# Kernel optimization log

Hardware: AMD Instinct MI355X
Metric: run time of the kernel (lower is better)

The kernel has to match this reference:

```python
import jax, jax.numpy as jnp
import numpy as np


def conv2d(x, w, b, pad):
    out = jax.lax.conv_general_dilated(x, w, (1, 1), ((pad, pad), (pad, pad)),
                                       dimension_numbers=('NCHW', 'OIHW', 'NCHW'))
    return out + b[None, :, None, None]


def silu(x):
    return x * jax.nn.sigmoid(x)


def group_norm(x, g, b, groups, eps=1e-5):
    B, C, H, W = x.shape
    xg = x.reshape(B, groups, C // groups, H, W)
    m = xg.mean(axis=(2, 3, 4), keepdims=True)
    v = xg.var(axis=(2, 3, 4), keepdims=True)
    xg = (xg - m) * jax.lax.rsqrt(v + eps)
    return xg.reshape(B, C, H, W) * g[None, :, None, None] + b[None, :, None, None]


def snake_cumsum(off):
    # off: [B,K,H,W]. Center kernel point has zero offset; points accumulate
    # outward from center (the 'snake' bend), as in DSCNet.
    K = off.shape[1]
    c = K // 2
    upper = jnp.cumsum(off[:, c + 1:], axis=1)
    lower = jnp.flip(jnp.cumsum(jnp.flip(off[:, :c], axis=1), axis=1), axis=1)
    return jnp.concatenate([lower, jnp.zeros_like(off[:, :1]), upper], axis=1)


def bilinear_gather(img, ys, xs):
    # img [B,C,H,W]; ys,xs [B,K,H,W] float coords -> sampled [B,C,K,H,W]
    B, C, H, W = img.shape
    K = ys.shape[1]
    ys = jnp.clip(ys, 0.0, H - 1.0)
    xs = jnp.clip(xs, 0.0, W - 1.0)
    y0f = jnp.floor(ys)
    x0f = jnp.floor(xs)
    wy = (ys - y0f)[:, None]  # [B,1,K,H,W]
    wx = (xs - x0f)[:, None]
    y0 = y0f.astype(jnp.int32)
    x0 = x0f.astype(jnp.int32)
    y1 = jnp.minimum(y0 + 1, H - 1)
    x1 = jnp.minimum(x0 + 1, W - 1)
    flat = img.reshape(B, C, H * W)

    def gat(yi, xi):
        idx = (yi * W + xi).reshape(B, -1)  # [B, K*H*W]
        g = jnp.take_along_axis(flat, idx[:, None, :], axis=2)
        return g.reshape(B, C, K, H, W)

    return (gat(y0, x0) * (1 - wy) * (1 - wx) + gat(y0, x1) * (1 - wy) * wx
            + gat(y1, x0) * wy * (1 - wx) + gat(y1, x1) * wy * wx)


def dsconv(x, off_w, off_b, dsc_w, dsc_b, gn_g, gn_b, morph, extend_scope=1.0):
    # Dynamic snake conv for one morphology.
    # morph 0: kernel spreads along x, bends in y; morph 1: opposite.
    B, C, H, W = x.shape
    K = dsc_w.shape[-1]
    c = K // 2
    off = jnp.tanh(conv2d(x, off_w, off_b, pad=1))  # [B,2K,H,W]; BN folded into conv bias
    bend = snake_cumsum(off[:, :K] if morph == 0 else off[:, K:])  # [B,K,H,W]
    spread = (jnp.arange(K) - c).astype(x.dtype)[None, :, None, None]
    hh = jnp.arange(H, dtype=x.dtype)[None, None, :, None]
    ww = jnp.arange(W, dtype=x.dtype)[None, None, None, :]
    if morph == 0:
        ys = hh + extend_scope * bend
        xs = jnp.broadcast_to(ww + spread, ys.shape)
    else:
        xs = ww + extend_scope * bend
        ys = jnp.broadcast_to(hh + spread, xs.shape)
    sampled = bilinear_gather(x, ys, xs)  # [B,C,K,H,W]
    # k-point conv over the stacked snake axis == (K,1)/(1,K) conv with stride K
    out = jnp.einsum('bckhw,ock->bohw', sampled, dsc_w) + dsc_b[None, :, None, None]
    O = dsc_w.shape[0]
    return jax.nn.relu(group_norm(out, gn_g, gn_b, groups=O // 4))


def dysnake_conv(x, p):
    # DySnakeConv: standard conv + snake-x + snake-y, concat, 1x1 fuse
    kpad = p['conv0_w'].shape[-1] // 2
    a = silu(conv2d(x, p['conv0_w'], p['conv0_b'], pad=kpad))
    bx = dsconv(x, p['offx_w'], p['offx_b'], p['dscx_w'], p['dscx_b'], p['gnx_g'], p['gnx_b'], morph=0)
    by = dsconv(x, p['offy_w'], p['offy_b'], p['dscy_w'], p['dscy_b'], p['gny_g'], p['gny_b'], morph=1)
    cat = jnp.concatenate([a, bx, by], axis=1)  # [B,3*ouc,H,W]
    return silu(jnp.einsum('bchw,oc->bohw', cat, p['fuse_w']) + p['fuse_b'][None, :, None, None])


_PNAMES = ['conv0_w', 'conv0_b', 'offx_w', 'offx_b', 'dscx_w', 'dscx_b', 'gnx_g', 'gnx_b',
           'offy_w', 'offy_b', 'dscy_w', 'dscy_b', 'gny_g', 'gny_b', 'fuse_w', 'fuse_b']


def setup_inputs() -> dict:
    key = jax.random.key(0)
    ks = iter(jax.random.split(key, 64))

    def rn(shape, s=0.05):
        return jax.random.normal(next(ks), shape, dtype=jnp.float32) * s

    B, H, W = 8, 80, 80
    c1, c2, c_ = 256, 256, 128
    kk = 3

    def block(inc, ouc, pre):
        return {
            pre + 'conv0_w': rn((ouc, inc, kk, kk)), pre + 'conv0_b': rn((ouc,)),
            pre + 'offx_w': rn((2 * kk, inc, 3, 3)), pre + 'offx_b': rn((2 * kk,)),
            pre + 'dscx_w': rn((ouc, inc, kk)), pre + 'dscx_b': rn((ouc,)),
            pre + 'gnx_g': jnp.ones((ouc,), jnp.float32), pre + 'gnx_b': jnp.zeros((ouc,), jnp.float32),
            pre + 'offy_w': rn((2 * kk, inc, 3, 3)), pre + 'offy_b': rn((2 * kk,)),
            pre + 'dscy_w': rn((ouc, inc, kk)), pre + 'dscy_b': rn((ouc,)),
            pre + 'gny_g': jnp.ones((ouc,), jnp.float32), pre + 'gny_b': jnp.zeros((ouc,), jnp.float32),
            pre + 'fuse_w': rn((ouc, 3 * ouc)), pre + 'fuse_b': rn((ouc,)),
        }

    inp = {'x': jax.random.normal(next(ks), (B, c1, H, W), dtype=jnp.float32)}
    inp.update(block(c1, c_, 'cv1_'))
    inp.update(block(c_, c2, 'cv2_'))
    return inp


def reference(x, cv1_conv0_w, cv1_conv0_b, cv1_offx_w, cv1_offx_b, cv1_dscx_w, cv1_dscx_b,
              cv1_gnx_g, cv1_gnx_b, cv1_offy_w, cv1_offy_b, cv1_dscy_w, cv1_dscy_b,
              cv1_gny_g, cv1_gny_b, cv1_fuse_w, cv1_fuse_b,
              cv2_conv0_w, cv2_conv0_b, cv2_offx_w, cv2_offx_b, cv2_dscx_w, cv2_dscx_b,
              cv2_gnx_g, cv2_gnx_b, cv2_offy_w, cv2_offy_b, cv2_dscy_w, cv2_dscy_b,
              cv2_gny_g, cv2_gny_b, cv2_fuse_w, cv2_fuse_b):
    p1 = dict(zip(_PNAMES, (cv1_conv0_w, cv1_conv0_b, cv1_offx_w, cv1_offx_b, cv1_dscx_w, cv1_dscx_b,
                            cv1_gnx_g, cv1_gnx_b, cv1_offy_w, cv1_offy_b, cv1_dscy_w, cv1_dscy_b,
                            cv1_gny_g, cv1_gny_b, cv1_fuse_w, cv1_fuse_b)))
    p2 = dict(zip(_PNAMES, (cv2_conv0_w, cv2_conv0_b, cv2_offx_w, cv2_offx_b, cv2_dscx_w, cv2_dscx_b,
                            cv2_gnx_g, cv2_gnx_b, cv2_offy_w, cv2_offy_b, cv2_dscy_w, cv2_dscy_b,
                            cv2_gny_g, cv2_gny_b, cv2_fuse_w, cv2_fuse_b)))
    h = dysnake_conv(x, p1)
    h = dysnake_conv(h, p2)
    return x + h  # shortcut and c1 == c2
```

## Files before the change

kernel.cpp:

```cpp
#include <hip/hip_runtime.h>
#include <cstddef>

#define B_   8
#define H_   80
#define W_   80
#define HW   6400

typedef __attribute__((ext_vector_type(8)))  short short8;
typedef __attribute__((ext_vector_type(16))) float f32x16;

__device__ __forceinline__ float bf2f(ushort u) {
    return __uint_as_float(((unsigned)u) << 16);
}
__device__ __forceinline__ ushort f2bf(float f) {
    unsigned u = __float_as_uint(f);
    u += 0x7FFF + ((u >> 16) & 1);
    return (ushort)(u >> 16);
}
__device__ __forceinline__ f32x16 mfma16(short8 a, short8 b, f32x16 c) {
    return __builtin_amdgcn_mfma_f32_32x32x16_bf16(a, b, c, 0, 0, 0);
}
__device__ __forceinline__ void async16(const void* g, void* l) {
    __builtin_amdgcn_global_load_lds(
        (const __attribute__((address_space(1))) unsigned int*)g,
        (__attribute__((address_space(3))) unsigned int*)l, 16, 0, 0);
}
__device__ __forceinline__ const ushort* frag_ptr(const ushort* sbuf, int row, int c8l) {
    return sbuf + row * 64 + ((c8l ^ (row & 7)) << 3);
}

__global__ __launch_bounds__(256) void transpose_x_kernel(
    const float* __restrict__ x, ushort* __restrict__ xh, int C) {
    __shared__ float s[64][65];
    int hw0 = blockIdx.x * 64, c0 = blockIdx.y * 64, b = blockIdx.z;
    int t = threadIdx.x;
    int hl = t & 63, cq = t >> 6;
    #pragma unroll
    for (int i = 0; i < 16; i++) {
        int cl = cq * 16 + i;
        s[cl][hl] = x[((size_t)(b * C + c0 + cl)) * HW + hw0 + hl];
    }
    __syncthreads();
    int cl = t & 63, hq = t >> 6;
    #pragma unroll
    for (int i = 0; i < 16; i++) {
        int hl2 = hq * 16 + i;
        xh[((size_t)(b * HW + hw0 + hl2)) * C + c0 + cl] = f2bf(s[cl][hl2]);
    }
}

__global__ __launch_bounds__(256) void final_add_kernel(
    const float* __restrict__ x, const ushort* __restrict__ h2,
    float* __restrict__ out, int C) {
    __shared__ float s[64][65];
    int hw0 = blockIdx.x * 64, c0 = blockIdx.y * 64, b = blockIdx.z;
    int t = threadIdx.x;
    int cl = t & 63, hq = t >> 6;
    #pragma unroll
    for (int i = 0; i < 16; i++) {
        int hl = hq * 16 + i;
        s[cl][hl] = bf2f(h2[((size_t)(b * HW + hw0 + hl)) * C + c0 + cl]);
    }
    __syncthreads();
    int hl = t & 63, cq = t >> 6;
    #pragma unroll
    for (int i = 0; i < 16; i++) {
        int cl2 = cq * 16 + i;
        size_t o = ((size_t)(b * C + c0 + cl2)) * HW + hw0 + hl;
        out[o] = x[o] + s[cl2][hl];
    }
}

__global__ void wprep_kernel(const float* __restrict__ src,
                             ushort* __restrict__ dst, int OC, int CIN, int T) {
    int idx = blockIdx.x * 256 + threadIdx.x;
    if (idx >= OC * CIN * T) return;
    int oc = idx / (CIN * T);
    int r = idx - oc * CIN * T;
    int ci = r / T, t_ = r - ci * T;
    dst[((size_t)oc * T + t_) * CIN + ci] = f2bf(src[idx]);
}

__global__ void wprep_off_kernel(const float* __restrict__ wx_,
                                 const float* __restrict__ bx_,
                                 const float* __restrict__ wy_,
                                 const float* __restrict__ by_,
                                 ushort* __restrict__ dst,
                                 float* __restrict__ bdst, int CIN) {
    int idx = blockIdx.x * 256 + threadIdx.x;
    if (idx < 4) {
        const int chs[4] = {0, 2, 3, 5};
        bdst[idx] = (idx < 2) ? bx_[chs[idx]] : by_[chs[idx]];
    }
    if (idx >= 32 * 9 * CIN) return;
    int oc = idx / (9 * CIN);
    int r = idx - oc * 9 * CIN;
    int tap = r / CIN, ci = r - tap * CIN;
    float v = 0.f;
    if (oc < 4) {
        const int chs[4] = {0, 2, 3, 5};
        const float* src = (oc < 2) ? wx_ : wy_;
        v = src[((size_t)chs[oc] * CIN + ci) * 9 + tap];
    }
    dst[idx] = f2bf(v);
}

__global__ __launch_bounds__(256, 2) void off_conv_mfma_kernel(
    const ushort* __restrict__ xh, const ushort* __restrict__ wB,
    const float* __restrict__ bias, float* __restrict__ off4, int CIN) {
    __shared__ ushort s_x[162 * 64];
    __shared__ ushort s_w[144 * 64];
    int tid = threadIdx.x;
    int ty0 = (blockIdx.x / 5) * 16, tx0 = (blockIdx.x % 5) * 16;
    int b = blockIdx.y;
    int lane = tid & 63, wid = tid >> 6;
    int l31 = lane & 31, kg = lane >> 5;
    int pym[2], pxm[2];
    #pragma unroll
    for (int mf = 0; mf < 2; mf++) {
        int p = wid * 64 + mf * 32 + l31;
        pym[mf] = p >> 4; pxm[mf] = p & 15;
    }
    f32x16 acc[2] = {};
    for (int c0 = 0; c0 < CIN; c0 += 32) {
        __syncthreads();
        for (int u = tid; u < 1296; u += 256) {
            int pid = u >> 2, ci8 = u & 3;
            int r = pid / 18, c = pid - r * 18;
            int gy = ty0 + r - 1, gx = tx0 + c - 1;
            uint4 v = make_uint4(0, 0, 0, 0);
            if ((unsigned)gy < H_ && (unsigned)gx < W_)
                v = *(const uint4*)(xh + ((size_t)(b * HW + gy * W_ + gx)) * CIN + c0 + ci8 * 8);
            int row = pid >> 1;
            int phys = (((pid & 1) << 2) + ci8) ^ (row & 7);
            *(uint4*)(s_x + row * 64 + phys * 8) = v;
        }
        for (int cc = wid; cc < 18; cc += 4) {
            int L = cc * 64 + lane;
            int row = L >> 3, phys = L & 7;
            int logical = phys ^ (row & 7);
            int tap = row >> 4, ocp = row & 15;
            int oc = ocp * 2 + (logical >> 2), ci8 = logical & 3;
            async16(wB + ((size_t)oc * 9 + tap) * CIN + c0 + ci8 * 8,
                    s_w + (size_t)L * 8);
        }
        __syncthreads();
        #pragma unroll
        for (int tap = 0; tap < 9; tap++) {
            int dy = tap / 3, dx = tap - dy * 3;
            int wrow = tap * 16 + (l31 >> 1);
            #pragma unroll
            for (int ks = 0; ks < 2; ks++) {
                int blk = ks * 2 + kg;
                int wphys = (((l31 & 1) << 2) + blk) ^ (wrow & 7);
                short8 bfr = *(const short8*)(s_w + wrow * 64 + wphys * 8);
                #pragma unroll
                for (int mf = 0; mf < 2; mf++) {
                    int pix = (pym[mf] + dy) * 18 + (pxm[mf] + dx);
                    int xrow = pix >> 1;
                    int xphys = (((pix & 1) << 2) + blk) ^ (xrow & 7);
                    short8 afr = *(const short8*)(s_x + xrow * 64 + xphys * 8);
                    acc[mf] = mfma16(afr, bfr, acc[mf]);
                }
            }
        }
    }
    int oc = l31;
    if (oc < 4) {
        float bb = bias[oc];
        #pragma unroll
        for (int mf = 0; mf < 2; mf++) {
            #pragma unroll
            for (int reg = 0; reg < 16; reg++) {
                int row = (reg & 3) + 8 * (reg >> 2) + 4 * kg;
                int p = wid * 64 + mf * 32 + row;
                int y = ty0 + (p >> 4), x = tx0 + (p & 15);
                off4[((size_t)b * 4 + oc) * HW + y * W_ + x] = tanhf(acc[mf][reg] + bb);
            }
        }
    }
}

__global__ __launch_bounds__(256, 2) void conv3x3_mfma_kernel(
    const ushort* __restrict__ xh, const ushort* __restrict__ wB,
    const float* __restrict__ bias, ushort* __restrict__ out,
    int CIN, int OC) {
    __shared__ ushort s_x[162 * 64];
    __shared__ ushort s_w[288 * 64];
    int tid = threadIdx.x;
    int ty0 = (blockIdx.x / 5) * 16, tx0 = (blockIdx.x % 5) * 16;
    int n0 = blockIdx.y * 64, b = blockIdx.z;
    int lane = tid & 63, wid = tid >> 6;
    int l31 = lane & 31, kg = lane >> 5;
    int wm = wid >> 1, wn = wid & 1;
    int pym[4], pxm[4];
    #pragma unroll
    for (int mf = 0; mf < 4; mf++) {
        int p = wm * 128 + mf * 32 + l31;
        pym[mf] = p >> 4; pxm[mf] = p & 15;
    }
    f32x16 acc[4] = {};
    for (int c0 = 0; c0 < CIN; c0 += 32) {
        __syncthreads();
        for (int u = tid; u < 1296; u += 256) {
            int pid = u >> 2, ci8 = u & 3;
            int r = pid / 18, c = pid - r * 18;
            int gy = ty0 + r - 1, gx = tx0 + c - 1;
            uint4 v = make_uint4(0, 0, 0, 0);
            if ((unsigned)gy < H_ && (unsigned)gx < W_)
                v = *(const uint4*)(xh + ((size_t)(b * HW + gy * W_ + gx)) * CIN + c0 + ci8 * 8);
            int row = pid >> 1;
            int phys = (((pid & 1) << 2) + ci8) ^ (row & 7);
            *(uint4*)(s_x + row * 64 + phys * 8) = v;
        }
        #pragma unroll
        for (int j = 0; j < 9; j++) {
            int L = (wid * 9 + j) * 64 + lane;
            int row = L >> 3, phys = L & 7;
            int logical = phys ^ (row & 7);
            int tap = row >> 5, ocp = row & 31;
            int oc = ocp * 2 + (logical >> 2), ci8 = logical & 3;
            async16(wB + ((size_t)(n0 + oc) * 9 + tap) * CIN + c0 + ci8 * 8,
                    s_w + (size_t)L * 8);
        }
        __syncthreads();
        #pragma unroll
        for (int tap = 0; tap < 9; tap++) {
            int dy = tap / 3, dx = tap - dy * 3;
            int ocl = wn * 32 + l31;
            int wrow = tap * 32 + (ocl >> 1);
            #pragma unroll
            for (int ks = 0; ks < 2; ks++) {
                int blk = ks * 2 + kg;
                int wphys = (((ocl & 1) << 2) + blk) ^ (wrow & 7);
                short8 bfr = *(const short8*)(s_w + wrow * 64 + wphys * 8);
                #pragma unroll
                for (int mf = 0; mf < 4; mf++) {
                    int pix = (pym[mf] + dy) * 18 + (pxm[mf] + dx);
                    int xrow = pix >> 1;
                    int xphys = (((pix & 1) << 2) + blk) ^ (xrow & 7);
                    short8 afr = *(const short8*)(s_x + xrow * 64 + xphys * 8);
                    acc[mf] = mfma16(afr, bfr, acc[mf]);
                }
            }
        }
    }
    int oc = n0 + wn * 32 + l31;
    float bb = bias[oc];
    #pragma unroll
    for (int mf = 0; mf < 4; mf++) {
        #pragma unroll
        for (int reg = 0; reg < 16; reg++) {
            int row = (reg & 3) + 8 * (reg >> 2) + 4 * kg;
            int p = wm * 128 + mf * 32 + row;
            int y = ty0 + (p >> 4), x = tx0 + (p & 15);
            float v = acc[mf][reg] + bb;
            v = v / (1.f + expf(-v));
            out[((size_t)(b * HW + y * W_ + x)) * OC + oc] = f2bf(v);
        }
    }
}

__global__ __launch_bounds__(256, 4) void dsc_gemm_kernel(
    const ushort* __restrict__ xh, const float* __restrict__ off4,
    const ushort* __restrict__ Bwx, const float* __restrict__ biasx,
    ushort* __restrict__ outx,
    const ushort* __restrict__ Bwy, const float* __restrict__ biasy,
    ushort* __restrict__ outy, float* __restrict__ stat, int CIN, int OC) {
    __shared__ ushort s_a[128 * 64];
    __shared__ ushort s_b[128 * 64];
    __shared__ int   s_i0[3][128];
    __shared__ int   s_i1[3][128];
    __shared__ float s_wl[3][128];
    int tid = threadIdx.x;
    int morph = blockIdx.z;
    const ushort* Bw = morph ? Bwy : Bwx;
    const float* bias = morph ? biasy : biasx;
    ushort* out = morph ? outy : outx;
    float* statm = stat + (size_t)morph * B_ * 256 * 2;
    int m0 = blockIdx.x * 128, n0 = blockIdx.y * 128;
    int b = m0 / HW, hw0 = m0 - b * HW;
    for (int u = tid; u < 384; u += 256) {
        int k3 = u >> 7, r = u & 127;
        int hw = hw0 + r;
        int h = hw / W_, w = hw - h * W_;
        float bend = 0.f;
        if (k3 != 1) {
            int mp = (morph ? 2 : 0) + (k3 >> 1);
            bend = off4[((size_t)b * 4 + mp) * HW + hw];
        }
        int i0, i1; float wl;
        if (morph == 0) {
            float ys = fminf(fmaxf((float)h + bend, 0.f), 79.f);
            float y0f = floorf(ys); wl = ys - y0f;
            int y0 = (int)y0f, y1 = min(y0 + 1, 79);
            int xk = min(max(w + k3 - 1, 0), 79);
            i0 = y0 * W_ + xk; i1 = y1 * W_ + xk;
        } else {
            float xs = fminf(fmaxf((float)w + bend, 0.f), 79.f);
            float x0f = floorf(xs); wl = xs - x0f;
            int x0 = (int)x0f, x1 = min(x0 + 1, 79);
            int yk = min(max(h + k3 - 1, 0), 79);
            i0 = yk * W_ + x0; i1 = yk * W_ + x1;
        }
        s_i0[k3][r] = i0; s_i1[k3][r] = i1; s_wl[k3][r] = wl;
    }
    int lane = tid & 63, wid = tid >> 6;
    int l31 = lane & 31, kg = lane >> 5;
    int wm = wid >> 1, wn = wid & 1;
    f32x16 acc[2][2] = {};
    int K = 3 * CIN, nk = K >> 6;
    const ushort* xb = xh + (size_t)b * HW * CIN;
    for (int kc = 0; kc < nk; kc++) {
        int kg64 = kc << 6;
        int k3 = kg64 / CIN;
        int cioff = kg64 - k3 * CIN;
        __syncthreads();
        #pragma unroll
        for (int j = 0; j < 4; j++) {
            int s = (wid * 4 + j) * 64 + lane;
            int r = s >> 3, c8p = s & 7;
            int c8l = c8p ^ (r & 7);
            async16(Bw + (size_t)(n0 + r) * K + kg64 + c8l * 8, s_b + s * 8);
        }
        #pragma unroll
        for (int i = 0; i < 4; i++) {
            int s = i * 256 + tid;
            int r = s >> 3, c8p = s & 7;
            int c8l = c8p ^ (r & 7);
            int ci = cioff + c8l * 8;
            float wl = s_wl[k3][r];
            uint4 u0 = *(const uint4*)(xb + (size_t)s_i0[k3][r] * CIN + ci);
            uint4 u1 = *(const uint4*)(xb + (size_t)s_i1[k3][r] * CIN + ci);
            const ushort* p0 = (const ushort*)&u0;
            const ushort* p1 = (const ushort*)&u1;
            ushort tv[8];
            #pragma unroll
            for (int j = 0; j < 8; j++) {
                float f0 = bf2f(p0[j]);
                tv[j] = f2bf(f0 + (bf2f(p1[j]) - f0) * wl);
            }
            *(uint4*)(s_a + s * 8) = *(uint4*)tv;
        }
        __syncthreads();
        #pragma unroll
        for (int ks = 0; ks < 4; ks++) {
            int c8l = ks * 2 + kg;
            short8 af0 = *(const short8*)frag_ptr(s_a, wm * 64 + l31, c8l);
            short8 af1 = *(const short8*)frag_ptr(s_a, wm * 64 + 32 + l31, c8l);
            short8 bf0 = *(const short8*)frag_ptr(s_b, wn * 64 + l31, c8l);
            short8 bf1 = *(const short8*)frag_ptr(s_b, wn * 64 + 32 + l31, c8l);
            acc[0][0] = mfma16(af0, bf0, acc[0][0]);
            acc[0][1] = mfma16(af0, bf1, acc[0][1]);
            acc[1][0] = mfma16(af1, bf0, acc[1][0]);
            acc[1][1] = mfma16(af1, bf1, acc[1][1]);
        }
    }
    #pragma unroll
    for (int nf = 0; nf < 2; nf++) {
        int n = n0 + wn * 64 + nf * 32 + l31;
        float bb = bias[n];
        float ssum = 0.f, ssq = 0.f;
        #pragma unroll
        for (int mf = 0; mf < 2; mf++) {
            #pragma unroll
            for (int reg = 0; reg < 16; reg++) {
                int row = (reg & 3) + 8 * (reg >> 2) + 4 * kg;
                int m = m0 + wm * 64 + mf * 32 + row;
                float v = acc[mf][nf][reg] + bb;
                ssum += v; ssq += v * v;
                out[(size_t)m * OC + n] = f2bf(v);
            }
        }
        ssum += __shfl_xor(ssum, 32);
        ssq  += __shfl_xor(ssq, 32);
        if (kg == 0) {
            float* st = statm + ((size_t)b * OC + n) * 2;
            atomicAdd(st, ssum);
            atomicAdd(st + 1, ssq);
        }
    }
}

__global__ __launch_bounds__(256, 4) void gemm128_kernel(
    const ushort* __restrict__ a0, const ushort* __restrict__ a1,
    const ushort* __restrict__ a2, int part_k,
    const ushort* __restrict__ Bw, int K, int N,
    const float* __restrict__ bias, ushort* __restrict__ out, int epi_silu) {
    __shared__ ushort s_a[128 * 64];
    __shared__ ushort s_b[128 * 64];
    int tid = threadIdx.x;
    int m0 = blockIdx.x * 128, n0 = blockIdx.y * 128;
    int lane = tid & 63, wid = tid >> 6;
    int l31 = lane & 31, kg = lane >> 5;
    int wm = wid >> 1, wn = wid & 1;
    f32x16 acc[2][2] = {};
    int nk = K >> 6;
    for (int kc = 0; kc < nk; kc++) {
        int kg64 = kc << 6;
        int part = kg64 / part_k;
        int koff = kg64 - part * part_k;
        const ushort* ap = (part == 0) ? a0 : (part == 1 ? a1 : a2);
        __syncthreads();
        #pragma unroll
        for (int j = 0; j < 4; j++) {
            int s = (wid * 4 + j) * 64 + lane;
            int r = s >> 3, c8p = s & 7;
            int c8l = c8p ^ (r & 7);
            async16(ap + (size_t)(m0 + r) * part_k + koff + c8l * 8, s_a + s * 8);
            async16(Bw + (size_t)(n0 + r) * K + kg64 + c8l * 8, s_b + s * 8);
        }
        __syncthreads();
        #pragma unroll
        for (int ks = 0; ks < 4; ks++) {
            int c8l = ks * 2 + kg;
            short8 af0 = *(const short8*)frag_ptr(s_a, wm * 64 + l31, c8l);
            short8 af1 = *(const short8*)frag_ptr(s_a, wm * 64 + 32 + l31, c8l);
            short8 bf0 = *(const short8*)frag_ptr(s_b, wn * 64 + l31, c8l);
            short8 bf1 = *(const short8*)frag_ptr(s_b, wn * 64 + 32 + l31, c8l);
            acc[0][0] = mfma16(af0, bf0, acc[0][0]);
            acc[0][1] = mfma16(af0, bf1, acc[0][1]);
            acc[1][0] = mfma16(af1, bf0, acc[1][0]);
            acc[1][1] = mfma16(af1, bf1, acc[1][1]);
        }
    }
    #pragma unroll
    for (int nf = 0; nf < 2; nf++) {
        int n = n0 + wn * 64 + nf * 32 + l31;
        float bb = bias[n];
        #pragma unroll
        for (int mf = 0; mf < 2; mf++) {
            #pragma unroll
            for (int reg = 0; reg < 16; reg++) {
                int row = (reg & 3) + 8 * (reg >> 2) + 4 * kg;
                int m = m0 + wm * 64 + mf * 32 + row;
                float v = acc[mf][nf][reg] + bb;
                if (epi_silu) v = v / (1.f + expf(-v));
                out[(size_t)m * N + n] = f2bf(v);
            }
        }
    }
}

__global__ void gn_finalize_kernel(const float* __restrict__ stat,
                                   const float* __restrict__ gx,
                                   const float* __restrict__ bx,
                                   const float* __restrict__ gy,
                                   const float* __restrict__ by,
                                   float* __restrict__ scx, float* __restrict__ shx,
                                   float* __restrict__ scy, float* __restrict__ shy,
                                   int C) {
    int idx = blockIdx.x * 256 + threadIdx.x;
    if (idx >= B_ * C) return;
    int which = blockIdx.y;
    const float* gamma = which ? gy : gx;
    const float* beta  = which ? by : bx;
    float* sc = which ? scy : scx;
    float* sh = which ? shy : shx;
    int b = idx / C, c = idx - b * C;
    const float* st = stat + (size_t)which * B_ * 256 * 2
                    + ((size_t)b * C + (c & ~3)) * 2;
    float s  = st[0] + st[2] + st[4] + st[6];
    float sq = st[1] + st[3] + st[5] + st[7];
    float mean = s / (4.f * HW);
    float var = sq / (4.f * HW) - mean * mean;
    float rs = rsqrtf(var + 1e-5f);
    float scale = rs * gamma[c];
    sc[idx] = scale;
    sh[idx] = beta[c] - mean * scale;
}

__global__ __launch_bounds__(256) void gn_apply_kernel(
    ushort* __restrict__ bqx, ushort* __restrict__ bqy,
    const float* __restrict__ scx, const float* __restrict__ shx,
    const float* __restrict__ scy, const float* __restrict__ shy, int C) {
    ushort* bq = blockIdx.y ? bqy : bqx;
    const float* sc = blockIdx.y ? scy : scx;
    const float* sh = blockIdx.y ? shy : shx;
    size_t e = ((size_t)blockIdx.x * 256 + threadIdx.x) * 8;
    int c = (int)(e % C);
    int b = (int)(e / ((size_t)HW * C));
    const float* scb = sc + (size_t)b * C + c;
    const float* shb = sh + (size_t)b * C + c;
    uint4 v = *(const uint4*)(bq + e);
    const ushort* sv = (const ushort*)&v;
    ushort tv[8];
    #pragma unroll
    for (int j = 0; j < 8; j++)
        tv[j] = f2bf(fmaxf(bf2f(sv[j]) * scb[j] + shb[j], 0.f));
    *(uint4*)(bq + e) = *(uint4*)tv;
}

struct BlkBuf {
    ushort *xh, *abuf, *bqx, *bqy, *hout;
    float *off4, *stat, *scx, *shx, *scy, *shy, *boff;
    ushort *wc, *wdx, *wdy, *wf, *woff;
};

static void run_block(const BlkBuf& B, int CIN, int OC,
                      const float* const* P, hipStream_t stream) {
    dim3 blk(256);
    hipMemsetAsync(B.stat, 0, (size_t)2 * B_ * 256 * 2 * 4, stream);
    off_conv_mfma_kernel<<<dim3(25, B_), blk, 0, stream>>>(
        B.xh, B.woff, B.boff, B.off4, CIN);
    conv3x3_mfma_kernel<<<dim3(25, OC / 64, B_), blk, 0, stream>>>(
        B.xh, B.wc, P[1], B.abuf, CIN, OC);
    dsc_gemm_kernel<<<dim3(400, OC / 128, 2), blk, 0, stream>>>(
        B.xh, B.off4, B.wdx, P[5], B.bqx, B.wdy, P[11], B.bqy, B.stat, CIN, OC);
    int fgrid = (B_ * OC + 255) / 256;
    gn_finalize_kernel<<<dim3(fgrid, 2), blk, 0, stream>>>(
        B.stat, P[6], P[7], P[12], P[13], B.scx, B.shx, B.scy, B.shy, OC);
    gn_apply_kernel<<<dim3((B_ * HW * OC) / 2048, 2), blk, 0, stream>>>(
        B.bqx, B.bqy, B.scx, B.shx, B.scy, B.shy, OC);
    gemm128_kernel<<<dim3(400, OC / 128), blk, 0, stream>>>(
        B.abuf, B.bqx, B.bqy, OC, B.wf, 3 * OC, OC, P[15], B.hout, 1);
}

extern "C" void kernel_launch(void* const* d_in, const int* in_sizes, int n_in,
                              void* d_out, int out_size, void* d_ws, size_t ws_size,
                              hipStream_t stream) {
    const float* x = (const float*)d_in[0];
    const float* P1[16];
    const float* P2[16];
    for (int i = 0; i < 16; i++) {
        P1[i] = (const float*)d_in[1 + i];
        P2[i] = (const float*)d_in[17 + i];
    }
    char* base = (char*)d_ws;
    size_t off = 0;
    auto alloc = [&](size_t bytes) -> char* {
        off = (off + 255) & ~(size_t)255;
        char* p = base + off;
        off += bytes;
        return p;
    };
    ushort* xh   = (ushort*)alloc((size_t)B_ * HW * 256 * 2);
    ushort* abuf = (ushort*)alloc((size_t)B_ * HW * 256 * 2);
    ushort* bqx  = (ushort*)alloc((size_t)B_ * HW * 256 * 2);
    ushort* bqy  = (ushort*)alloc((size_t)B_ * HW * 256 * 2);
    ushort* h1   = (ushort*)alloc((size_t)B_ * HW * 128 * 2);
    float*  off4 = (float*)alloc((size_t)B_ * 4 * HW * 4);
    float*  stat = (float*)alloc((size_t)2 * B_ * 256 * 2 * 4);
    float*  scx  = (float*)alloc(B_ * 256 * 4);
    float*  shx  = (float*)alloc(B_ * 256 * 4);
    float*  scy  = (float*)alloc(B_ * 256 * 4);
    float*  shy  = (float*)alloc(B_ * 256 * 4);
    ushort* wc1  = (ushort*)alloc((size_t)128 * 9 * 256 * 2);
    ushort* wc2  = (ushort*)alloc((size_t)256 * 9 * 128 * 2);
    ushort* wdx1 = (ushort*)alloc((size_t)128 * 3 * 256 * 2);
    ushort* wdy1 = (ushort*)alloc((size_t)128 * 3 * 256 * 2);
    ushort* wdx2 = (ushort*)alloc((size_t)256 * 3 * 128 * 2);
    ushort* wdy2 = (ushort*)alloc((size_t)256 * 3 * 128 * 2);
    ushort* wf1  = (ushort*)alloc((size_t)128 * 384 * 2);
    ushort* wf2  = (ushort*)alloc((size_t)256 * 768 * 2);
    ushort* wo1  = (ushort*)alloc((size_t)32 * 9 * 256 * 2);
    ushort* wo2  = (ushort*)alloc((size_t)32 * 9 * 128 * 2);
    float*  bo1  = (float*)alloc(32 * 4);
    float*  bo2  = (float*)alloc(32 * 4);

    dim3 blk(256);
    auto wp = [&](const float* s, ushort* d, int OC, int CIN, int T) {
        int n = OC * CIN * T;
        wprep_kernel<<<(n + 255) / 256, blk, 0, stream>>>(s, d, OC, CIN, T);
    };
    wp(P1[0], wc1, 128, 256, 9);
    wp(P1[4], wdx1, 128, 256, 3);
    wp(P1[10], wdy1, 128, 256, 3);
    wp(P1[14], wf1, 128, 384, 1);
    wp(P2[0], wc2, 256, 128, 9);
    wp(P2[4], wdx2, 256, 128, 3);
    wp(P2[10], wdy2, 256, 128, 3);
    wp(P2[14], wf2, 256, 768, 1);
    wprep_off_kernel<<<(32 * 9 * 256 + 255) / 256, blk, 0, stream>>>(
        P1[2], P1[3], P1[8], P1[9], wo1, bo1, 256);
    wprep_off_kernel<<<(32 * 9 * 128 + 255) / 256, blk, 0, stream>>>(
        P2[2], P2[3], P2[8], P2[9], wo2, bo2, 128);

    transpose_x_kernel<<<dim3(100, 4, B_), blk, 0, stream>>>(x, xh, 256);

    BlkBuf B1 = {xh, abuf, bqx, bqy, h1, off4, stat, scx, shx, scy, shy,
                 bo1, wc1, wdx1, wdy1, wf1, wo1};
    run_block(B1, 256, 128, P1, stream);

    ushort* h2 = xh;
    BlkBuf B2 = {h1, abuf, bqx, bqy, h2, off4, stat, scx, shx, scy, shy,
                 bo2, wc2, wdx2, wdy2, wf2, wo2};
    run_block(B2, 128, 256, P2, stream);

    final_add_kernel<<<dim3(100, 4, B_), blk, 0, stream>>>(x, h2, (float*)d_out, 256);
}
```

Before: 572.2 us.

## Zero-pad NHWC activations and run conv3x3 as implicit GEMM with async loads

Activations are stored in a zero-padded 82x82 NHWC buffer so convolution halo loads need no bounds checks. The 3x3 conv is rewritten as a 128x128 implicit GEMM that streams both operands straight into LDS with global_load_lds over a 9*CIN reduction, replacing the spatial-tile kernel that reused one input halo across all taps. Producer kernels write into the padded interior, and two memsets clear the borders. The trade-off is that input tiles are reloaded once per tap instead of being reused from shared memory, and the buffers grow slightly.

```diff
diff --git a/kernel.cpp b/kernel.cpp
--- a/kernel.cpp
+++ b/kernel.cpp
@@ -5,6 +5,8 @@
 #define H_   80
 #define W_   80
 #define HW   6400
+#define W2   82
+#define HW2  6724
 
 typedef __attribute__((ext_vector_type(8)))  short short8;
 typedef __attribute__((ext_vector_type(16))) float f32x16;
@@ -30,7 +32,7 @@
 }
 
 __global__ __launch_bounds__(256) void transpose_x_kernel(
-    const float* __restrict__ x, ushort* __restrict__ xh, int C) {
+    const float* __restrict__ x, ushort* __restrict__ xp, int C) {
     __shared__ float s[64][65];
     int hw0 = blockIdx.x * 64, c0 = blockIdx.y * 64, b = blockIdx.z;
     int t = threadIdx.x;
@@ -45,7 +47,9 @@
     #pragma unroll
     for (int i = 0; i < 16; i++) {
         int hl2 = hq * 16 + i;
-        xh[((size_t)(b * HW + hw0 + hl2)) * C + c0 + cl] = f2bf(s[cl][hl2]);
+        int hw = hw0 + hl2;
+        int h = hw / W_, w = hw - h * W_;
+        xp[((size_t)(b * HW2 + (h + 1) * W2 + w + 1)) * C + c0 + cl] = f2bf(s[cl][hl2]);
     }
 }
 
@@ -106,7 +110,7 @@
 }
 
 __global__ __launch_bounds__(256, 2) void off_conv_mfma_kernel(
-    const ushort* __restrict__ xh, const ushort* __restrict__ wB,
+    const ushort* __restrict__ xp, const ushort* __restrict__ wB,
     const float* __restrict__ bias, float* __restrict__ off4, int CIN) {
     __shared__ ushort s_x[162 * 64];
     __shared__ ushort s_w[144 * 64];
@@ -127,10 +131,9 @@
         for (int u = tid; u < 1296; u += 256) {
             int pid = u >> 2, ci8 = u & 3;
             int r = pid / 18, c = pid - r * 18;
-            int gy = ty0 + r - 1, gx = tx0 + c - 1;
-            uint4 v = make_uint4(0, 0, 0, 0);
-            if ((unsigned)gy < H_ && (unsigned)gx < W_)
-                v = *(const uint4*)(xh + ((size_t)(b * HW + gy * W_ + gx)) * CIN + c0 + ci8 * 8);
+            int py = ty0 + r, px = tx0 + c;
+            uint4 v = *(const uint4*)(xp + ((size_t)(b * HW2 + py * W2 + px)) * CIN
+                                      + c0 + ci8 * 8);
             int row = pid >> 1;
             int phys = (((pid & 1) << 2) + ci8) ^ (row & 7);
             *(uint4*)(s_x + row * 64 + phys * 8) = v;
@@ -181,88 +184,81 @@
     }
 }
 
-__global__ __launch_bounds__(256, 2) void conv3x3_mfma_kernel(
-    const ushort* __restrict__ xh, const ushort* __restrict__ wB,
+__global__ __launch_bounds__(256, 4) void conv3x3_gemm_kernel(
+    const ushort* __restrict__ xp, const ushort* __restrict__ wB,
     const float* __restrict__ bias, ushort* __restrict__ out,
     int CIN, int OC) {
-    __shared__ ushort s_x[162 * 64];
-    __shared__ ushort s_w[288 * 64];
+    __shared__ ushort s_a[128 * 64];
+    __shared__ ushort s_b[128 * 64];
     int tid = threadIdx.x;
-    int ty0 = (blockIdx.x / 5) * 16, tx0 = (blockIdx.x % 5) * 16;
-    int n0 = blockIdx.y * 64, b = blockIdx.z;
+    int m0 = blockIdx.x * 128, n0 = blockIdx.y * 128;
+    int b = m0 / HW, hw0 = m0 - b * HW;
     int lane = tid & 63, wid = tid >> 6;
     int l31 = lane & 31, kg = lane >> 5;
     int wm = wid >> 1, wn = wid & 1;
-    int pym[4], pxm[4];
-    #pragma unroll
-    for (int mf = 0; mf < 4; mf++) {
-        int p = wm * 128 + mf * 32 + l31;
-        pym[mf] = p >> 4; pxm[mf] = p & 15;
-    }
-    f32x16 acc[4] = {};
-    for (int c0 = 0; c0 < CIN; c0 += 32) {
-        __syncthreads();
-        for (int u = tid; u < 1296; u += 256) {
-            int pid = u >> 2, ci8 = u & 3;
-            int r = pid / 18, c = pid - r * 18;
-            int gy = ty0 + r - 1, gx = tx0 + c - 1;
-            uint4 v = make_uint4(0, 0, 0, 0);
-            if ((unsigned)gy < H_ && (unsigned)gx < W_)
-                v = *(const uint4*)(xh + ((size_t)(b * HW + gy * W_ + gx)) * CIN + c0 + ci8 * 8);
-            int row = pid >> 1;
-            int phys = (((pid & 1) << 2) + ci8) ^ (row & 7);
-            *(uint4*)(s_x + row * 64 + phys * 8) = v;
-        }
-        #pragma unroll
-        for (int j = 0; j < 9; j++) {
-            int L = (wid * 9 + j) * 64 + lane;
-            int row = L >> 3, phys = L & 7;
-            int logical = phys ^ (row & 7);
-            int tap = row >> 5, ocp = row & 31;
-            int oc = ocp * 2 + (logical >> 2), ci8 = logical & 3;
-            async16(wB + ((size_t)(n0 + oc) * 9 + tap) * CIN + c0 + ci8 * 8,
-                    s_w + (size_t)L * 8);
-        }
-        __syncthreads();
-        #pragma unroll
-        for (int tap = 0; tap < 9; tap++) {
-            int dy = tap / 3, dx = tap - dy * 3;
-            int ocl = wn * 32 + l31;
-            int wrow = tap * 32 + (ocl >> 1);
+    const ushort* xpb = xp + (size_t)b * HW2 * CIN;
+    const ushort* asrc[4];
+    #pragma unroll
+    for (int j = 0; j < 4; j++) {
+        int s = (wid * 4 + j) * 64 + lane;
+        int r = s >> 3, c8p = s & 7;
+        int c8l = c8p ^ (r & 7);
+        int hw = hw0 + r;
+        int h = hw / W_, w = hw - h * W_;
+        asrc[j] = xpb + ((size_t)((h + 1) * W2 + (w + 1))) * CIN + c8l * 8;
+    }
+    f32x16 acc[2][2] = {};
+    int K = 9 * CIN, nk = K >> 6;
+    int tap = 0, cioff = 0;
+    for (int kc = 0; kc < nk; kc++) {
+        int kg64 = kc << 6;
+        int dy = tap / 3, dx = tap - dy * 3;
+        int soff = ((dy - 1) * W2 + (dx - 1)) * CIN + cioff;
+        __syncthreads();
+        #pragma unroll
+        for (int j = 0; j < 4; j++) {
+            int s = (wid * 4 + j) * 64 + lane;
+            int r = s >> 3, c8p = s & 7;
+            int c8l = c8p ^ (r & 7);
+            async16(wB + (size_t)(n0 + r) * K + kg64 + c8l * 8, s_b + s * 8);
+            async16(asrc[j] + soff, s_a + s * 8);
+        }
+        __syncthreads();
+        #pragma unroll
+        for (int ks = 0; ks < 4; ks++) {
+            int c8l = ks * 2 + kg;
+            short8 af0 = *(const short8*)frag_ptr(s_a, wm * 64 + l31, c8l);
+            short8 af1 = *(const short8*)frag_ptr(s_a, wm * 64 + 32 + l31, c8l);
+            short8 bf0 = *(const short8*)frag_ptr(s_b, wn * 64 + l31, c8l);
+            short8 bf1 = *(const short8*)frag_ptr(s_b, wn * 64 + 32 + l31, c8l);
+            acc[0][0] = mfma16(af0, bf0, acc[0][0]);
+            acc[0][1] = mfma16(af0, bf1, acc[0][1]);
+            acc[1][0] = mfma16(af1, bf0, acc[1][0]);
+            acc[1][1] = mfma16(af1, bf1, acc[1][1]);
+        }
+        cioff += 64;
+        if (cioff == CIN) { cioff = 0; tap++; }
+    }
+    #pragma unroll
+    for (int nf = 0; nf < 2; nf++) {
+        int n = n0 + wn * 64 + nf * 32 + l31;
+        float bb = bias[n];
+        #pragma unroll
+        for (int mf = 0; mf < 2; mf++) {
             #pragma unroll
-            for (int ks = 0; ks < 2; ks++) {
-                int blk = ks * 2 + kg;
-                int wphys = (((ocl & 1) << 2) + blk) ^ (wrow & 7);
-                short8 bfr = *(const short8*)(s_w + wrow * 64 + wphys * 8);
-                #pragma unroll
-                for (int mf = 0; mf < 4; mf++) {
-                    int pix = (pym[mf] + dy) * 18 + (pxm[mf] + dx);
-                    int xrow = pix >> 1;
-                    int xphys = (((pix & 1) << 2) + blk) ^ (xrow & 7);
-                    short8 afr = *(const short8*)(s_x + xrow * 64 + xphys * 8);
-                    acc[mf] = mfma16(afr, bfr, acc[mf]);
-                }
+            for (int reg = 0; reg < 16; reg++) {
+                int row = (reg & 3) + 8 * (reg >> 2) + 4 * kg;
+                int m = m0 + wm * 64 + mf * 32 + row;
+                float v = acc[mf][nf][reg] + bb;
+                v = v / (1.f + expf(-v));
+                out[(size_t)m * OC + n] = f2bf(v);
             }
         }
     }
-    int oc = n0 + wn * 32 + l31;
-    float bb = bias[oc];
-    #pragma unroll
-    for (int mf = 0; mf < 4; mf++) {
-        #pragma unroll
-        for (int reg = 0; reg < 16; reg++) {
-            int row = (reg & 3) + 8 * (reg >> 2) + 4 * kg;
-            int p = wm * 128 + mf * 32 + row;
-            int y = ty0 + (p >> 4), x = tx0 + (p & 15);
-            float v = acc[mf][reg] + bb;
-            v = v / (1.f + expf(-v));
-            out[((size_t)(b * HW + y * W_ + x)) * OC + oc] = f2bf(v);
-        }
-    }
 }
 
 __global__ __launch_bounds__(256, 4) void dsc_gemm_kernel(
-    const ushort* __restrict__ xh, const float* __restrict__ off4,
+    const ushort* __restrict__ xp, const float* __restrict__ off4,
     const ushort* __restrict__ Bwx, const float* __restrict__ biasx,
     ushort* __restrict__ outx,
     const ushort* __restrict__ Bwy, const float* __restrict__ biasy,
@@ -295,13 +291,13 @@
             float y0f = floorf(ys); wl = ys - y0f;
             int y0 = (int)y0f, y1 = min(y0 + 1, 79);
             int xk = min(max(w + k3 - 1, 0), 79);
-            i0 = y0 * W_ + xk; i1 = y1 * W_ + xk;
+            i0 = (y0 + 1) * W2 + xk + 1; i1 = (y1 + 1) * W2 + xk + 1;
         } else {
             float xs = fminf(fmaxf((float)w + bend, 0.f), 79.f);
             float x0f = floorf(xs); wl = xs - x0f;
             int x0 = (int)x0f, x1 = min(x0 + 1, 79);
             int yk = min(max(h + k3 - 1, 0), 79);
-            i0 = yk * W_ + x0; i1 = yk * W_ + x1;
+            i0 = (yk + 1) * W2 + x0 + 1; i1 = (yk + 1) * W2 + x1 + 1;
         }
         s_i0[k3][r] = i0; s_i1[k3][r] = i1; s_wl[k3][r] = wl;
     }
@@ -310,7 +306,7 @@
     int wm = wid >> 1, wn = wid & 1;
     f32x16 acc[2][2] = {};
     int K = 3 * CIN, nk = K >> 6;
-    const ushort* xb = xh + (size_t)b * HW * CIN;
+    const ushort* xb = xp + (size_t)b * HW2 * CIN;
     for (int kc = 0; kc < nk; kc++) {
         int kg64 = kc << 6;
         int k3 = kg64 / CIN;
@@ -386,7 +382,8 @@
     const ushort* __restrict__ a0, const ushort* __restrict__ a1,
     const ushort* __restrict__ a2, int part_k,
     const ushort* __restrict__ Bw, int K, int N,
-    const float* __restrict__ bias, ushort* __restrict__ out, int epi_silu) {
+    const float* __restrict__ bias, ushort* __restrict__ out, int epi_silu,
+    int out_pad) {
     __shared__ ushort s_a[128 * 64];
     __shared__ ushort s_b[128 * 64];
     int tid = threadIdx.x;
@@ -436,7 +433,13 @@
                 int m = m0 + wm * 64 + mf * 32 + row;
                 float v = acc[mf][nf][reg] + bb;
                 if (epi_silu) v = v / (1.f + expf(-v));
-                out[(size_t)m * N + n] = f2bf(v);
+                size_t mm = (size_t)m;
+                if (out_pad) {
+                    int bb_ = m / HW, hw = m - bb_ * HW;
+                    int h = hw / W_, w = hw - h * W_;
+                    mm = (size_t)bb_ * HW2 + (h + 1) * W2 + w + 1;
+                }
+                out[mm * N + n] = f2bf(v);
             }
         }
     }
@@ -492,28 +495,28 @@
 }
 
 struct BlkBuf {
-    ushort *xh, *abuf, *bqx, *bqy, *hout;
+    ushort *xp, *abuf, *bqx, *bqy, *hout;
     float *off4, *stat, *scx, *shx, *scy, *shy, *boff;
     ushort *wc, *wdx, *wdy, *wf, *woff;
 };
 
 static void run_block(const BlkBuf& B, int CIN, int OC,
-                      const float* const* P, hipStream_t stream) {
+                      const float* const* P, int out_pad, hipStream_t stream) {
     dim3 blk(256);
     hipMemsetAsync(B.stat, 0, (size_t)2 * B_ * 256 * 2 * 4, stream);
     off_conv_mfma_kernel<<<dim3(25, B_), blk, 0, stream>>>(
-        B.xh, B.woff, B.boff, B.off4, CIN);
-    conv3x3_mfma_kernel<<<dim3(25, OC / 64, B_), blk, 0, stream>>>(
-        B.xh, B.wc, P[1], B.abuf, CIN, OC);
+        B.xp, B.woff, B.boff, B.off4, CIN);
+    conv3x3_gemm_kernel<<<dim3(B_ * HW / 128, OC / 128), blk, 0, stream>>>(
+        B.xp, B.wc, P[1], B.abuf, CIN, OC);
     dsc_gemm_kernel<<<dim3(400, OC / 128, 2), blk, 0, stream>>>(
-        B.xh, B.off4, B.wdx, P[5], B.bqx, B.wdy, P[11], B.bqy, B.stat, CIN, OC);
+        B.xp, B.off4, B.wdx, P[5], B.bqx, B.wdy, P[11], B.bqy, B.stat, CIN, OC);
     int fgrid = (B_ * OC + 255) / 256;
     gn_finalize_kernel<<<dim3(fgrid, 2), blk, 0, stream>>>(
         B.stat, P[6], P[7], P[12], P[13], B.scx, B.shx, B.scy, B.shy, OC);
     gn_apply_kernel<<<dim3((B_ * HW * OC) / 2048, 2), blk, 0, stream>>>(
         B.bqx, B.bqy, B.scx, B.shx, B.scy, B.shy, OC);
     gemm128_kernel<<<dim3(400, OC / 128), blk, 0, stream>>>(
-        B.abuf, B.bqx, B.bqy, OC, B.wf, 3 * OC, OC, P[15], B.hout, 1);
+        B.abuf, B.bqx, B.bqy, OC, B.wf, 3 * OC, OC, P[15], B.hout, 1, out_pad);
 }
 
 extern "C" void kernel_launch(void* const* d_in, const int* in_sizes, int n_in,
@@ -534,11 +537,11 @@
         off += bytes;
         return p;
     };
-    ushort* xh   = (ushort*)alloc((size_t)B_ * HW * 256 * 2);
+    ushort* xp1  = (ushort*)alloc((size_t)B_ * HW2 * 256 * 2);
+    ushort* xp2  = (ushort*)alloc((size_t)B_ * HW2 * 128 * 2);
     ushort* abuf = (ushort*)alloc((size_t)B_ * HW * 256 * 2);
     ushort* bqx  = (ushort*)alloc((size_t)B_ * HW * 256 * 2);
     ushort* bqy  = (ushort*)alloc((size_t)B_ * HW * 256 * 2);
-    ushort* h1   = (ushort*)alloc((size_t)B_ * HW * 128 * 2);
     float*  off4 = (float*)alloc((size_t)B_ * 4 * HW * 4);
     float*  stat = (float*)alloc((size_t)2 * B_ * 256 * 2 * 4);
     float*  scx  = (float*)alloc(B_ * 256 * 4);
@@ -557,6 +560,10 @@
     ushort* wo2  = (ushort*)alloc((size_t)32 * 9 * 128 * 2);
     float*  bo1  = (float*)alloc(32 * 4);
     float*  bo2  = (float*)alloc(32 * 4);
+    ushort* h2 = xp1;
+
+    hipMemsetAsync(xp1, 0, (size_t)B_ * HW2 * 256 * 2, stream);
+    hipMemsetAsync(xp2, 0, (size_t)B_ * HW2 * 128 * 2, stream);
 
     dim3 blk(256);
     auto wp = [&](const float* s, ushort* d, int OC, int CIN, int T) {
@@ -576,16 +583,15 @@
     wprep_off_kernel<<<(32 * 9 * 128 + 255) / 256, blk, 0, stream>>>(
         P2[2], P2[3], P2[8], P2[9], wo2, bo2, 128);
 
-    transpose_x_kernel<<<dim3(100, 4, B_), blk, 0, stream>>>(x, xh, 256);
-
-    BlkBuf B1 = {xh, abuf, bqx, bqy, h1, off4, stat, scx, shx, scy, shy,
+    transpose_x_kernel<<<dim3(100, 4, B_), blk, 0, stream>>>(x, xp1, 256);
+
+    BlkBuf B1 = {xp1, abuf, bqx, bqy, xp2, off4, stat, scx, shx, scy, shy,
                  bo1, wc1, wdx1, wdy1, wf1, wo1};
-    run_block(B1, 256, 128, P1, stream);
-
-    ushort* h2 = xh;
-    BlkBuf B2 = {h1, abuf, bqx, bqy, h2, off4, stat, scx, shx, scy, shy,
+    run_block(B1, 256, 128, P1, 1, stream);
+
+    BlkBuf B2 = {xp2, abuf, bqx, bqy, h2, off4, stat, scx, shx, scy, shy,
                  bo2, wc2, wdx2, wdy2, wf2, wo2};
-    run_block(B2, 128, 256, P2, stream);
+    run_block(B2, 128, 256, P2, 0, stream);
 
     final_add_kernel<<<dim3(100, 4, B_), blk, 0, stream>>>(x, h2, (float*)d_out, 256);
 }
```

New measurement: 584.1 us. +2.1%, slower.
